# Kernel tuning notes

Hardware: AMD Instinct MI355X
Metric: run time of the kernel (lower is better)

Reference implementation:

```python
import jax, jax.numpy as jnp
import numpy as np

B, S, D, DOM, L = 16, 512, 512, 8, 3  # batch, seq_len, mem_dim (S==D required by outputs*rel), domains, layers


def setup_inputs() -> dict:
    key = jax.random.key(0)
    ks = jax.random.split(key, 16)
    adj = jax.random.uniform(ks[0], (B, S, S), jnp.float32)
    rel = jax.random.uniform(ks[1], (B, S, S), jnp.float32)
    gcn_inputs = jax.random.normal(ks[2], (B, S, D), jnp.float32)
    frontrel = jax.random.normal(ks[3], (B, S, D), jnp.float32)
    backrel = jax.random.normal(ks[4], (B, S, D), jnp.float32)
    # depmap: exactly one selected column per (b, row) so masked_select reshapes to [B,S]
    depmap = jax.nn.one_hot(jax.random.randint(ks[5], (B, S), 0, S), S, dtype=jnp.float32)
    dom_idx = jax.random.randint(ks[6], (B, S), 0, DOM)
    has_dom = jax.random.bernoulli(ks[7], 0.5, (B, S)).astype(jnp.float32)
    domain_id = jax.nn.one_hot(dom_idx, DOM, dtype=jnp.float32) * has_dom[..., None]
    redom_idx = jax.random.randint(ks[8], (B, S), 0, DOM)
    has_re = jax.random.bernoulli(ks[9], 0.5, (B, S)).astype(jnp.float32)
    redomain_id = jax.nn.one_hot(redom_idx, DOM, dtype=jnp.float32) * has_re[..., None]
    domain = jax.random.bernoulli(ks[10], 0.5, (B, S, DOM, 1))
    mask = jnp.ones((B, S), dtype=bool)
    sc = 1.0 / np.sqrt(D)
    W_layers = jax.random.normal(ks[11], (L, D, D), jnp.float32) * sc
    b_layers = jnp.zeros((L, D), jnp.float32)
    prelu_a = jnp.full((L,), 0.25, jnp.float32)  # nn.PReLU default
    W_dg = jax.random.normal(ks[12], (D, D), jnp.float32) * sc
    b_dg = jnp.zeros((D,), jnp.float32)
    W_mg = jax.random.normal(ks[13], (2 * D, D), jnp.float32) * (1.0 / np.sqrt(2 * D))
    b_mg = jnp.zeros((D,), jnp.float32)
    W_out = jax.random.normal(ks[14], (L * D, D), jnp.float32) * (1.0 / np.sqrt(L * D))
    b_out = jnp.zeros((D,), jnp.float32)
    return dict(adj=adj, domain=domain, domain_id=domain_id, redomain_id=redomain_id,
                frontrel=frontrel, backrel=backrel, depmap=depmap, rel=rel,
                gcn_inputs=gcn_inputs, mask=mask, W_layers=W_layers, b_layers=b_layers,
                prelu_a=prelu_a, W_dg=W_dg, b_dg=b_dg, W_mg=W_mg, b_mg=b_mg,
                W_out=W_out, b_out=b_out)


def _forward(adj, domain, domain_id, redomain_id, frontrel, backrel, depmap, rel,
             gcn_inputs, W_layers, b_layers, prelu_a, W_dg, b_dg, W_mg, b_mg, W_out, b_out):
    denom = jnp.sum(adj, axis=2, keepdims=True) + 1.0                     # [B,S,1]
    domain_mask = jnp.sum(domain_id, axis=-1, keepdims=True) == 1.0       # [B,S,1]
    redomain_mask = jnp.sum(redomain_id, axis=-1, keepdims=True) == 1.0   # [B,S,1]
    frontadj = jnp.sum(adj * depmap, axis=-1)                             # [B,S]
    backadj = jnp.sum(jnp.swapaxes(adj, -1, -2) * depmap, axis=-1)        # [B,S]
    outputs = gcn_inputs
    outs = []
    for l in range(L):
        frontoutputs = jnp.where(domain_mask, 0.0, outputs)
        backoutputs = jnp.where(redomain_mask, 0.0, jnp.einsum('bij,bjd->bid', rel, outputs))
        # domain pooling: mask then max over sequence -> [B,DOM,D]
        pooled = jnp.max(jnp.where(domain, -10000.0, outputs[:, :, None, :]), axis=1)
        domain_outputs = jax.nn.sigmoid(pooled @ W_dg + b_dg)             # domain_gate
        frontoutputs = frontoutputs + jnp.einsum('bsk,bkd->bsd', domain_id, domain_outputs)
        backoutputs = backoutputs + jnp.einsum('bsk,bkd->bsd', redomain_id, domain_outputs)
        frontdepadj = jax.nn.sigmoid(jnp.concatenate([frontoutputs, frontrel], -1) @ W_mg + b_mg)
        backdepadj = jax.nn.sigmoid(jnp.concatenate([backoutputs, backrel], -1) @ W_mg + b_mg)
        delta = jnp.einsum('bji,bjd->bid', rel, frontadj[..., None] * frontdepadj * frontoutputs)
        delta = delta + backadj[..., None] * backdepadj * backoutputs
        Ax = jnp.einsum('bij,bjd->bid', adj, outputs * rel)               # requires S==D
        AxW = (Ax @ W_layers[l] + b_layers[l]) + (outputs @ W_layers[l] + b_layers[l]) + delta
        x = AxW / denom
        outputs = jnp.where(x >= 0, x, prelu_a[l] * x)                    # PReLU
        outs.append(outputs)                                              # dropout is eval-mode identity
    gcn_outputs = jnp.concatenate(outs, axis=2)                           # [B,S,L*D]
    return gcn_outputs @ W_out + b_out + gcn_inputs


def reference(adj, domain, domain_id, redomain_id, frontrel, backrel, depmap, rel,
              gcn_inputs, mask, W_layers, b_layers, prelu_a, W_dg, b_dg, W_mg, b_mg,
              W_out, b_out):
    return _forward(adj, domain, domain_id, redomain_id, frontrel, backrel, depmap, rel,
                    gcn_inputs, W_layers, b_layers, prelu_a, W_dg, b_dg, W_mg, b_mg,
                    W_out, b_out)
```

## Files before the change

### kernel.cpp

```cpp
#include <hip/hip_runtime.h>
#include <math.h>

#define SD_  (512*512)
#define BSD_ (16*512*512)

typedef unsigned short u16;
typedef short s16x8 __attribute__((ext_vector_type(8)));
typedef float f32x4 __attribute__((ext_vector_type(4)));

__device__ __forceinline__ float sigmoidf_(float x) { return 1.0f / (1.0f + __expf(-x)); }

__device__ __forceinline__ u16 f2bf(float f) {
    unsigned int u = __float_as_uint(f);
    u += 0x7fffu + ((u >> 16) & 1u);
    return (u16)(u >> 16);
}
__device__ __forceinline__ float bf2f(u16 h) { return __uint_as_float((unsigned)h << 16); }

__device__ __forceinline__ void glds16(const void* g, void* l) {
    __builtin_amdgcn_global_load_lds((const __attribute__((address_space(1))) unsigned int*)g,
                                     (__attribute__((address_space(3))) unsigned int*)l, 16, 0, 0);
}

struct GP {
    const u16 *A1, *A2;  int lda1, lda2;  long sA;
    const u16 *B1, *B2;  int bt1, bt2;  int ldb1, ldb2;  long sB;
    void *C1, *C2;  int obf1, obf2;  int ldc1, ldc2;  long sC;
    const void *Ci1, *Ci2;  int cbf1, cbf2;  int ldci1, ldci2;  long sCi1, sCi2;
    const float *bias;  float bS;
    const float *sc1, *sc2;
    const int *selm1, *seli1, *selm2, *seli2;
    const float *DG;
    const float *invden, *prelu;  int pidx;
    int M, K, zs, swzY;
};

template<int EPI, int ASEL>
__global__ __launch_bounds__(512, 2)
void gemm2(const GP p)
{
    __shared__ short LS[16384];
    const int tid = threadIdx.x;
    int bx, by, bz;
    if (p.swzY >= 0) {
        const int bid = blockIdx.x + 4 * (blockIdx.y + gridDim.y * blockIdx.z);
        const int ppx = (gridDim.y * gridDim.z) >> 3;
        const int xcd = bid & 7, idx = bid >> 3;
        const int pair = xcd * ppx + (idx >> 2);
        bx = idx & 3;
        by = pair & ((1 << p.swzY) - 1);
        bz = pair >> p.swzY;
    } else { bx = blockIdx.x; by = blockIdx.y; bz = blockIdx.z; }

    const int seg = (bz >= p.zs) ? 1 : 0;
    const int z = seg ? bz - p.zs : bz;
    const u16* Ab = (seg ? p.A2 : p.A1) + z * p.sA;
    const int lda = seg ? p.lda2 : p.lda1;
    const u16* Bb = (seg ? p.B2 : p.B1) + z * p.sB;
    const int bt  = seg ? p.bt2  : p.bt1;
    const int ldb = seg ? p.ldb2 : p.ldb1;

    const int m0 = by * 128, n0 = bx * 128;
    const int srow = ((tid >> 6) << 4) | (tid & 15);
    const int sk0 = ((tid >> 4) & 3) << 3;

    int aselv = 0; long dgoff = 0;
    if (ASEL) {
        const int* selm = seg ? p.selm2 : p.selm1;
        const int* seli = seg ? p.seli2 : p.seli1;
        const int row = m0 + srow;
        aselv = selm[row];
        dgoff = (long)((((row) >> 9) << 3) + seli[row]) * 512;
    }
    const u16* aRow = Ab + (long)(m0 + srow) * lda + sk0;
    const u16* bRowT = bt ? (Bb + (long)(n0 + srow) * ldb + sk0) : nullptr;

    auto stage = [&](int kk, int buf) {
        short* lsA = &LS[(buf << 13) + tid * 8];
        short* lsB = lsA + 4096;
        if (ASEL) {
            s16x8 v;
            if (aselv) {
                const float* dg = p.DG + dgoff + kk + sk0;
#pragma unroll
                for (int q = 0; q < 8; ++q) v[q] = (short)f2bf(dg[q]);
            } else v = *(const s16x8*)(aRow + kk);
            *(s16x8*)lsA = v;
        } else {
            glds16(aRow + kk, lsA);
        }
        if (bt) {
            glds16(bRowT + kk, lsB);
        } else {
            s16x8 v;
#pragma unroll
            for (int q = 0; q < 8; ++q) v[q] = (short)Bb[(long)(kk + sk0 + q) * ldb + n0 + srow];
            *(s16x8*)lsB = v;
        }
    };

    const int wave = tid >> 6, lane = tid & 63;
    const int rowSelA = (wave >> 2) << 2;
    const int rowSelB = (wave & 3) << 1;

    f32x4 acc[4][2] = {};
    stage(0, 0);
    const int nkb = p.K >> 5;
    for (int kb = 0; kb < nkb; ++kb) {
        __syncthreads();
        if (kb + 1 < nkb) stage((kb + 1) << 5, (kb + 1) & 1);
        const short* ls = &LS[(kb & 1) << 13];
        s16x8 aF[4], bF[2];
#pragma unroll
        for (int mt = 0; mt < 4; ++mt) aF[mt] = *(const s16x8*)&ls[((rowSelA + mt) * 64 + lane) * 8];
#pragma unroll
        for (int nt = 0; nt < 2; ++nt) bF[nt] = *(const s16x8*)&ls[4096 + ((rowSelB + nt) * 64 + lane) * 8];
#pragma unroll
        for (int mt = 0; mt < 4; ++mt)
#pragma unroll
            for (int nt = 0; nt < 2; ++nt)
                acc[mt][nt] = __builtin_amdgcn_mfma_f32_16x16x32_bf16(aF[mt], bF[nt], acc[mt][nt], 0, 0, 0);
    }

    const int ml = lane & 15, quad = lane >> 4;
    const int wm = (wave >> 2) * 64, wn = (wave & 3) * 32;
    u16* Cb16 = (u16*)(seg ? p.C2 : p.C1);
    float* Cb32 = (float*)(seg ? p.C2 : p.C1);
    const int obf = seg ? p.obf2 : p.obf1;
    const int ldc = seg ? p.ldc2 : p.ldc1;
    if (obf) Cb16 += z * p.sC; else Cb32 += z * p.sC;
    const u16* Ci16 = (const u16*)(seg ? p.Ci2 : p.Ci1);
    const float* Ci32 = (const float*)(seg ? p.Ci2 : p.Ci1);
    const int cbf = seg ? p.cbf2 : p.cbf1;
    const int ldci = seg ? p.ldci2 : p.ldci1;
    {
        const long sCi = seg ? p.sCi2 : p.sCi1;
        if (cbf) Ci16 += z * sCi; else Ci32 += z * sCi;
    }
    const float pal = (EPI == 4) ? p.prelu[p.pidx] : 0.0f;
    const float* scp = (EPI == 8) ? (seg ? p.sc2 : p.sc1) : nullptr;
    const int* eselm = (EPI == 8) ? (seg ? p.selm2 : p.selm1) : nullptr;
    const int* eseli = (EPI == 8) ? (seg ? p.seli2 : p.seli1) : nullptr;

#pragma unroll
    for (int mt = 0; mt < 4; ++mt) {
#pragma unroll
        for (int r = 0; r < 4; ++r) {
            const int row = m0 + wm + mt * 16 + quad * 4 + r;
            float idv = 1.0f, scv = 0.0f; int selv = 0; long dgrow = 0;
            if (EPI == 4) idv = p.invden[z * p.M + row];
            if (EPI == 8) {
                scv = scp[row]; selv = eselm[row];
                dgrow = (long)(((row >> 9) << 3) + eseli[row]) * 512;
            }
            const long crow = (long)row * ldc;
            const long cirow = (long)row * ldci;
#pragma unroll
            for (int nt = 0; nt < 2; ++nt) {
                const int col = n0 + wn + nt * 16 + ml;
                float x = acc[mt][nt][r];
                float cin = 0.0f;
                if (EPI == 3 || EPI == 4 || EPI == 7 || EPI == 8)
                    cin = cbf ? bf2f(Ci16[cirow + col]) : Ci32[cirow + col];
                if (EPI == 1) x += p.bias[col];
                else if (EPI == 3) x += cin;
                else if (EPI == 4) { x = (x + p.bS * p.bias[col] + cin) * idv; x = (x >= 0.0f) ? x : pal * x; }
                else if (EPI == 6) x = sigmoidf_(x + p.bias[col]);
                else if (EPI == 7) x += p.bias[col] + cin;
                else if (EPI == 8) {
                    const float av = selv ? p.DG[dgrow + col] : bf2f(Ab[(long)row * lda + col]);
                    x = sigmoidf_(x + cin) * scv * av;
                }
                if (obf) Cb16[crow + col] = f2bf(x); else Cb32[crow + col] = x;
            }
        }
    }
}

__global__ __launch_bounds__(256)
void cvt_k(const float* __restrict__ s, u16* __restrict__ d)
{
    const long i = ((long)blockIdx.x * 256 + threadIdx.x) * 4;
    const float4 v = *(const float4*)&s[i];
    ushort4 h = { f2bf(v.x), f2bf(v.y), f2bf(v.z), f2bf(v.w) };
    *(ushort4*)&d[i] = h;
}

__global__ __launch_bounds__(256)
void trcvt_k(const float* __restrict__ src, u16* __restrict__ dstT, u16* __restrict__ dstN,
             const int R, const int C, const long sS, const long sDT, const long sDN)
{
    __shared__ u16 t[64][72];
    const float* s = src + blockIdx.z * sS;
    const int r0 = blockIdx.y * 64, c0 = blockIdx.x * 64;
    const int tid = threadIdx.x;
    const int lr = tid >> 2, lc4 = (tid & 3) * 16;
#pragma unroll
    for (int j = 0; j < 4; ++j) {
        const float4 v = *(const float4*)&s[(long)(r0 + lr) * C + c0 + lc4 + j * 4];
        ushort4 h = { f2bf(v.x), f2bf(v.y), f2bf(v.z), f2bf(v.w) };
        *(ushort4*)&t[lr][lc4 + j * 4] = h;
        if (dstN) *(ushort4*)&dstN[blockIdx.z * sDN + (long)(r0 + lr) * C + c0 + lc4 + j * 4] = h;
    }
    __syncthreads();
    const int lcol = tid >> 2, rc = (tid & 3) * 16;
#pragma unroll
    for (int j = 0; j < 2; ++j) {
        s16x8 v;
#pragma unroll
        for (int q = 0; q < 8; ++q) v[q] = (short)t[rc + j * 8 + q][lcol];
        *(s16x8*)&dstT[blockIdx.z * sDT + (long)(c0 + lcol) * R + r0 + rc + j * 8] = v;
    }
}

__global__ __launch_bounds__(256)
void e0_k(const float* __restrict__ adj, const float* __restrict__ depmap,
          const float* __restrict__ domain_id, const float* __restrict__ redomain_id,
          float* __restrict__ invden, float* __restrict__ fa, int* __restrict__ dcol,
          int* __restrict__ dm, int* __restrict__ dsel, int* __restrict__ rm, int* __restrict__ rsel)
{
    const int bs = blockIdx.x;
    const int t = threadIdx.x;
    const float* arow = adj + (long)bs * 512;
    const float* drow = depmap + (long)bs * 512;
    __shared__ float red[256];
    __shared__ int scol;
    if (t == 0) scol = 0;
    const float a0 = arow[t], a1 = arow[t + 256];
    const float p0 = drow[t], p1 = drow[t + 256];
    if (p0 > 0.5f) scol = t;
    if (p1 > 0.5f) scol = t + 256;
    red[t] = a0 + a1;
    __syncthreads();
    for (int off = 128; off > 0; off >>= 1) { if (t < off) red[t] += red[t + off]; __syncthreads(); }
    if (t == 0) invden[bs] = 1.0f / (red[0] + 1.0f);
    __syncthreads();
    red[t] = a0 * p0 + a1 * p1;
    __syncthreads();
    for (int off = 128; off > 0; off >>= 1) { if (t < off) red[t] += red[t + off]; __syncthreads(); }
    if (t == 0) {
        fa[bs] = red[0];
        dcol[bs] = scol;
        const float* q = domain_id + (long)bs * 8;
        float s = 0.f; int sel = 0;
        for (int k = 0; k < 8; ++k) { float v = q[k]; s += v; if (v > 0.5f) sel = k; }
        dm[bs] = (s > 0.5f) ? 1 : 0; dsel[bs] = sel;
        const float* r = redomain_id + (long)bs * 8;
        s = 0.f; sel = 0;
        for (int k = 0; k < 8; ++k) { float v = r[k]; s += v; if (v > 0.5f) sel = k; }
        rm[bs] = (s > 0.5f) ? 1 : 0; rsel[bs] = sel;
    }
}

__global__ void e0b_k(const float* __restrict__ adj, const int* __restrict__ dcol, float* __restrict__ ba)
{
    const int bs = blockIdx.x * 256 + threadIdx.x;
    const int b = bs >> 9, s = bs & 511;
    ba[bs] = adj[((long)b * 512 + dcol[bs]) * 512 + s];
}

__global__ __launch_bounds__(256)
void pool1_k(const u16* __restrict__ OUT, const int ldO, const int* __restrict__ domain,
             const u16* __restrict__ relb, u16* __restrict__ cm, u16* __restrict__ OxRT)
{
    const int b = blockIdx.x >> 4, c = blockIdx.x & 15;
    const int s0 = c * 32, tid = threadIdx.x;
    __shared__ int dom[256];
    dom[tid] = domain[((long)(b * 512 + s0 + (tid >> 3))) * 8 + (tid & 7)];
    __syncthreads();
    const int d0 = tid * 2;
    float mxa[8], mxb[8];
#pragma unroll
    for (int k = 0; k < 8; ++k) { mxa[k] = -10000.0f; mxb[k] = -10000.0f; }
    s16x8 pA[4], pB[4];
#pragma unroll
    for (int s = 0; s < 32; ++s) {
        const int row = b * 512 + s0 + s;
        const unsigned uv = *(const unsigned*)&OUT[(long)row * ldO + d0];
        const unsigned rv = *(const unsigned*)&relb[(long)row * 512 + d0];
        const float vx = bf2f((u16)(uv & 0xffff)), vy = bf2f((u16)(uv >> 16));
        const float rx = bf2f((u16)(rv & 0xffff)), ry = bf2f((u16)(rv >> 16));
        pA[s >> 3][s & 7] = (short)f2bf(vx * rx);
        pB[s >> 3][s & 7] = (short)f2bf(vy * ry);
        const int* ds = &dom[s * 8];
#pragma unroll
        for (int k = 0; k < 8; ++k) {
            mxa[k] = fmaxf(mxa[k], ds[k] ? -10000.0f : vx);
            mxb[k] = fmaxf(mxb[k], ds[k] ? -10000.0f : vy);
        }
    }
#pragma unroll
    for (int j = 0; j < 4; ++j) *(s16x8*)&OxRT[((long)b * 512 + d0) * 512 + s0 + j * 8] = pA[j];
#pragma unroll
    for (int j = 0; j < 4; ++j) *(s16x8*)&OxRT[((long)b * 512 + d0 + 1) * 512 + s0 + j * 8] = pB[j];
#pragma unroll
    for (int k = 0; k < 8; ++k) {
        ushort2 h = { f2bf(mxa[k]), f2bf(mxb[k]) };
        *(ushort2*)&cm[((long)((b * 16 + c) * 8 + k)) * 512 + d0] = h;
    }
}

__global__ void pool2_k(const u16* __restrict__ cm, u16* __restrict__ pooled)
{
    const int q = blockIdx.x * 256 + threadIdx.x;
    const int b = q >> 12, k = (q >> 9) & 7, d = q & 511;
    float m = -1e30f;
    for (int c = 0; c < 16; ++c)
        m = fmaxf(m, bf2f(cm[((long)((b * 16 + c) * 8 + k)) * 512 + d]));
    pooled[((long)(b * 8 + k)) * 512 + d] = f2bf(m);
}

extern "C" void kernel_launch(void* const* d_in, const int* in_sizes, int n_in,
                              void* d_out, int out_size, void* d_ws, size_t ws_size,
                              hipStream_t stream)
{
    const float* adj         = (const float*)d_in[0];
    const int*   domain      = (const int*)d_in[1];
    const float* domain_id   = (const float*)d_in[2];
    const float* redomain_id = (const float*)d_in[3];
    const float* frontrel    = (const float*)d_in[4];
    const float* backrel     = (const float*)d_in[5];
    const float* depmap      = (const float*)d_in[6];
    const float* rel         = (const float*)d_in[7];
    const float* gcn         = (const float*)d_in[8];
    const float* W_layers    = (const float*)d_in[10];
    const float* b_layers    = (const float*)d_in[11];
    const float* prelu_a     = (const float*)d_in[12];
    const float* W_dg        = (const float*)d_in[13];
    const float* b_dg        = (const float*)d_in[14];
    const float* W_mg        = (const float*)d_in[15];
    const float* b_mg        = (const float*)d_in[16];
    const float* W_out       = (const float*)d_in[17];
    const float* b_out       = (const float*)d_in[18];
    float* out = (float*)d_out;

    char* w = (char*)d_ws;
    auto alloc = [&](size_t bytes) { void* p = (void*)w; w += (bytes + 255) & ~(size_t)255; return p; };
    const size_t Bb = (size_t)BSD_ * 2;
    u16* OUTS_bf = (u16*)alloc((size_t)8192 * 1536 * 2);
    u16* RB_bf   = (u16*)alloc(Bb);
    u16* XB_bf   = (u16*)alloc(Bb);
    u16* XF_bf   = (u16*)alloc(Bb);
    u16* OxRT_bf = (u16*)alloc(Bb);
    u16* DL_bf   = (u16*)alloc(Bb);
    u16* AXO_bf  = (u16*)alloc(Bb);
    u16* BB_bf   = (u16*)alloc(Bb);
    u16* FB_bf   = (u16*)alloc(Bb);
    u16* rel_bf  = (u16*)alloc(Bb);
    u16* relT_bf = (u16*)alloc(Bb);
    u16* adj_bf  = (u16*)alloc(Bb);
    u16* gcn_bf  = (u16*)alloc(Bb);
    u16* frel_bf = (u16*)alloc(Bb);
    u16* brel_bf = (u16*)alloc(Bb);
    u16* WmgT1 = (u16*)alloc((size_t)SD_ * 2);
    u16* WmgT2 = (u16*)alloc((size_t)SD_ * 2);
    u16* WdgT  = (u16*)alloc((size_t)SD_ * 2);
    u16* WlT   = (u16*)alloc((size_t)3 * SD_ * 2);
    u16* WoutT = (u16*)alloc((size_t)512 * 1536 * 2);
    u16* cm     = (u16*)alloc((size_t)16 * 16 * 8 * 512 * 2);
    u16* pooled = (u16*)alloc((size_t)16 * 8 * 512 * 2);
    float* DG     = (float*)alloc((size_t)16 * 8 * 512 * 4);
    float* invden = (float*)alloc(8192 * 4);
    float* fa     = (float*)alloc(8192 * 4);
    float* ba     = (float*)alloc(8192 * 4);
    int* dcol = (int*)alloc(8192 * 4);
    int* dm   = (int*)alloc(8192 * 4);
    int* dsel = (int*)alloc(8192 * 4);
    int* rm   = (int*)alloc(8192 * 4);
    int* rsel = (int*)alloc(8192 * 4);

    cvt_k<<<4096, 256, 0, stream>>>(adj, adj_bf);
    cvt_k<<<4096, 256, 0, stream>>>(gcn, gcn_bf);
    cvt_k<<<4096, 256, 0, stream>>>(frontrel, frel_bf);
    cvt_k<<<4096, 256, 0, stream>>>(backrel, brel_bf);
    trcvt_k<<<dim3(8, 8, 16), 256, 0, stream>>>(rel, relT_bf, rel_bf, 512, 512, SD_, SD_, SD_);
    trcvt_k<<<dim3(8, 8, 1), 256, 0, stream>>>(W_mg, WmgT1, nullptr, 512, 512, 0, 0, 0);
    trcvt_k<<<dim3(8, 8, 1), 256, 0, stream>>>(W_mg + SD_, WmgT2, nullptr, 512, 512, 0, 0, 0);
    trcvt_k<<<dim3(8, 8, 1), 256, 0, stream>>>(W_dg, WdgT, nullptr, 512, 512, 0, 0, 0);
    trcvt_k<<<dim3(8, 8, 3), 256, 0, stream>>>(W_layers, WlT, nullptr, 512, 512, SD_, SD_, 0);
    trcvt_k<<<dim3(8, 24, 1), 256, 0, stream>>>(W_out, WoutT, nullptr, 1536, 512, 0, 0, 0);
    e0_k<<<8192, 256, 0, stream>>>(adj, depmap, domain_id, redomain_id, invden, fa, dcol, dm, dsel, rm, rsel);
    e0b_k<<<32, 256, 0, stream>>>(adj, dcol, ba);

    const dim3 blk(512);

    {
        GP p{};
        p.A1 = brel_bf; p.A2 = frel_bf; p.lda1 = p.lda2 = 512; p.sA = 0;
        p.B1 = p.B2 = WmgT2; p.bt1 = p.bt2 = 1; p.ldb1 = p.ldb2 = 512; p.sB = 0;
        p.C1 = BB_bf; p.C2 = FB_bf; p.obf1 = p.obf2 = 1; p.ldc1 = p.ldc2 = 512; p.sC = 0;
        p.bias = b_mg; p.M = 8192; p.K = 512; p.zs = 1; p.swzY = 6;
        gemm2<1, 0><<<dim3(4, 64, 2), blk, 0, stream>>>(p);
    }

    for (int l = 0; l < 3; ++l) {
        const u16* OUTp = (l == 0) ? gcn_bf : (OUTS_bf + (l - 1) * 512);
        const int ldO = (l == 0) ? 512 : 1536;
        const long sO = (long)512 * ldO;

        {
            GP p{};
            p.A1 = rel_bf; p.lda1 = 512; p.sA = SD_;
            p.B1 = OUTp; p.bt1 = 0; p.ldb1 = ldO; p.sB = sO;
            p.C1 = RB_bf; p.obf1 = 1; p.ldc1 = 512; p.sC = SD_;
            p.M = 512; p.K = 512; p.zs = 16; p.swzY = 2;
            gemm2<0, 0><<<dim3(4, 4, 16), blk, 0, stream>>>(p);
        }
        pool1_k<<<256, 256, 0, stream>>>(OUTp, ldO, domain, rel_bf, cm, OxRT_bf);
        pool2_k<<<256, 256, 0, stream>>>(cm, pooled);
        {
            GP p{};
            p.A1 = pooled; p.lda1 = 512; p.B1 = WdgT; p.bt1 = 1; p.ldb1 = 512;
            p.C1 = DG; p.obf1 = 0; p.ldc1 = 512;
            p.bias = b_dg; p.M = 128; p.K = 512; p.zs = 1; p.swzY = -1;
            gemm2<6, 0><<<dim3(4, 1, 1), blk, 0, stream>>>(p);
        }
        {
            GP p{};
            p.A1 = RB_bf; p.lda1 = 512; p.A2 = OUTp; p.lda2 = ldO; p.sA = 0;
            p.selm1 = rm; p.seli1 = rsel; p.selm2 = dm; p.seli2 = dsel; p.DG = DG;
            p.B1 = p.B2 = WmgT1; p.bt1 = p.bt2 = 1; p.ldb1 = p.ldb2 = 512; p.sB = 0;
            p.Ci1 = BB_bf; p.Ci2 = FB_bf; p.cbf1 = p.cbf2 = 1; p.ldci1 = p.ldci2 = 512; p.sCi1 = p.sCi2 = 0;
            p.C1 = XB_bf; p.C2 = XF_bf; p.obf1 = p.obf2 = 1; p.ldc1 = p.ldc2 = 512; p.sC = 0;
            p.sc1 = ba; p.sc2 = fa; p.M = 8192; p.K = 512; p.zs = 1; p.swzY = 6;
            gemm2<8, 1><<<dim3(4, 64, 2), blk, 0, stream>>>(p);
        }
        {
            GP p{};
            p.A1 = relT_bf; p.lda1 = 512; p.A2 = adj_bf; p.lda2 = 512; p.sA = SD_;
            p.B1 = XF_bf; p.bt1 = 0; p.ldb1 = 512;
            p.B2 = OxRT_bf; p.bt2 = 1; p.ldb2 = 512; p.sB = SD_;
            p.Ci1 = XB_bf; p.cbf1 = 1; p.ldci1 = 512; p.sCi1 = SD_;
            p.Ci2 = OUTp; p.cbf2 = 1; p.ldci2 = ldO; p.sCi2 = sO;
            p.C1 = DL_bf; p.C2 = AXO_bf; p.obf1 = p.obf2 = 1; p.ldc1 = p.ldc2 = 512; p.sC = SD_;
            p.M = 512; p.K = 512; p.zs = 16; p.swzY = 2;
            gemm2<3, 0><<<dim3(4, 4, 32), blk, 0, stream>>>(p);
        }
        {
            GP p{};
            p.A1 = AXO_bf; p.lda1 = 512; p.sA = SD_;
            p.B1 = WlT + (long)l * SD_; p.bt1 = 1; p.ldb1 = 512; p.sB = 0;
            p.Ci1 = DL_bf; p.cbf1 = 1; p.ldci1 = 512; p.sCi1 = SD_;
            p.C1 = OUTS_bf + l * 512; p.obf1 = 1; p.ldc1 = 1536; p.sC = (long)512 * 1536;
            p.bias = b_layers + l * 512; p.bS = 2.0f;
            p.invden = invden; p.prelu = prelu_a; p.pidx = l;
            p.M = 512; p.K = 512; p.zs = 16; p.swzY = 2;
            gemm2<4, 0><<<dim3(4, 4, 16), blk, 0, stream>>>(p);
        }
    }

    {
        GP p{};
        p.A1 = OUTS_bf; p.lda1 = 1536; p.sA = 0;
        p.B1 = WoutT; p.bt1 = 1; p.ldb1 = 1536; p.sB = 0;
        p.Ci1 = gcn; p.cbf1 = 0; p.ldci1 = 512; p.sCi1 = 0;
        p.C1 = out; p.obf1 = 0; p.ldc1 = 512; p.sC = 0;
        p.bias = b_out; p.M = 8192; p.K = 1536; p.zs = 1; p.swzY = 6;
        gemm2<7, 0><<<dim3(4, 64, 1), blk, 0, stream>>>(p);
    }
}
```

Measured before the change: 712.1 us.

## Write transposed GEMM outputs so all B operands load via direct LDS

```diff
diff --git a/kernel.cpp b/kernel.cpp
--- a/kernel.cpp
+++ b/kernel.cpp
@@ -24,30 +24,31 @@
 
 struct GP {
     const u16 *A1, *A2;  int lda1, lda2;  long sA;
-    const u16 *B1, *B2;  int bt1, bt2;  int ldb1, ldb2;  long sB;
-    void *C1, *C2;  int obf1, obf2;  int ldc1, ldc2;  long sC;
-    const void *Ci1, *Ci2;  int cbf1, cbf2;  int ldci1, ldci2;  long sCi1, sCi2;
+    const u16 *B1, *B2;  int ldb1, ldb2;  long sB;
+    void *C1, *C2;  int obf1, obf2, ldc1, ldc2;  long sC;
+    u16 *CT1, *CT2;  int ldcT1, ldcT2;  long sCT;
+    const void *Ci1, *Ci2;  int cbf1, cbf2, ldci1, ldci2;  long sCi1, sCi2;
     const float *bias;  float bS;
     const float *sc1, *sc2;
     const int *selm1, *seli1, *selm2, *seli2;
     const float *DG;
     const float *invden, *prelu;  int pidx;
-    int M, K, zs, swzY;
+    int M, K, zs, swzX, swzY;
 };
 
-template<int EPI, int ASEL>
-__global__ __launch_bounds__(512, 2)
+template<int EPI, int ASEL, int TRW>
+__global__ __launch_bounds__(256, 4)
 void gemm2(const GP p)
 {
-    __shared__ short LS[16384];
+    __shared__ short LS[12288];
     const int tid = threadIdx.x;
     int bx, by, bz;
-    if (p.swzY >= 0) {
-        const int bid = blockIdx.x + 4 * (blockIdx.y + gridDim.y * blockIdx.z);
+    if (p.swzX >= 0) {
+        const int bid = blockIdx.x + gridDim.x * (blockIdx.y + gridDim.y * blockIdx.z);
         const int ppx = (gridDim.y * gridDim.z) >> 3;
         const int xcd = bid & 7, idx = bid >> 3;
-        const int pair = xcd * ppx + (idx >> 2);
-        bx = idx & 3;
+        const int pair = xcd * ppx + (idx >> p.swzX);
+        bx = idx & ((1 << p.swzX) - 1);
         by = pair & ((1 << p.swzY) - 1);
         bz = pair >> p.swzY;
     } else { bx = blockIdx.x; by = blockIdx.y; bz = blockIdx.z; }
@@ -57,51 +58,49 @@
     const u16* Ab = (seg ? p.A2 : p.A1) + z * p.sA;
     const int lda = seg ? p.lda2 : p.lda1;
     const u16* Bb = (seg ? p.B2 : p.B1) + z * p.sB;
-    const int bt  = seg ? p.bt2  : p.bt1;
     const int ldb = seg ? p.ldb2 : p.ldb1;
 
-    const int m0 = by * 128, n0 = bx * 128;
+    const int m0 = by * 128, n0 = bx * 64;
     const int srow = ((tid >> 6) << 4) | (tid & 15);
     const int sk0 = ((tid >> 4) & 3) << 3;
 
-    int aselv = 0; long dgoff = 0;
+    const u16* aRow0 = Ab + (long)(m0 + srow) * lda + sk0;
+    const u16* aRow1 = aRow0 + (long)64 * lda;
+    const u16* bRow  = Bb + (long)(n0 + srow) * ldb + sk0;
+
+    int aselv0 = 0, aselv1 = 0; long dgo0 = 0, dgo1 = 0;
     if (ASEL) {
         const int* selm = seg ? p.selm2 : p.selm1;
         const int* seli = seg ? p.seli2 : p.seli1;
-        const int row = m0 + srow;
-        aselv = selm[row];
-        dgoff = (long)((((row) >> 9) << 3) + seli[row]) * 512;
-    }
-    const u16* aRow = Ab + (long)(m0 + srow) * lda + sk0;
-    const u16* bRowT = bt ? (Bb + (long)(n0 + srow) * ldb + sk0) : nullptr;
+        const int r0 = m0 + srow, r1 = r0 + 64;
+        aselv0 = selm[r0]; dgo0 = (long)(((r0 >> 9) << 3) + seli[r0]) * 512 + sk0;
+        aselv1 = selm[r1]; dgo1 = (long)(((r1 >> 9) << 3) + seli[r1]) * 512 + sk0;
+    }
 
     auto stage = [&](int kk, int buf) {
-        short* lsA = &LS[(buf << 13) + tid * 8];
-        short* lsB = lsA + 4096;
+        short* base = &LS[buf * 6144];
         if (ASEL) {
-            s16x8 v;
-            if (aselv) {
-                const float* dg = p.DG + dgoff + kk + sk0;
-#pragma unroll
-                for (int q = 0; q < 8; ++q) v[q] = (short)f2bf(dg[q]);
-            } else v = *(const s16x8*)(aRow + kk);
-            *(s16x8*)lsA = v;
+            s16x8 v0, v1;
+            if (aselv0) { const float* dg = p.DG + dgo0 + kk;
+#pragma unroll
+                for (int q = 0; q < 8; ++q) v0[q] = (short)f2bf(dg[q]); }
+            else v0 = *(const s16x8*)(aRow0 + kk);
+            if (aselv1) { const float* dg = p.DG + dgo1 + kk;
+#pragma unroll
+                for (int q = 0; q < 8; ++q) v1[q] = (short)f2bf(dg[q]); }
+            else v1 = *(const s16x8*)(aRow1 + kk);
+            *(s16x8*)&base[tid * 8] = v0;
+            *(s16x8*)&base[2048 + tid * 8] = v1;
         } else {
-            glds16(aRow + kk, lsA);
-        }
-        if (bt) {
-            glds16(bRowT + kk, lsB);
-        } else {
-            s16x8 v;
-#pragma unroll
-            for (int q = 0; q < 8; ++q) v[q] = (short)Bb[(long)(kk + sk0 + q) * ldb + n0 + srow];
-            *(s16x8*)lsB = v;
-        }
+            glds16(aRow0 + kk, &base[tid * 8]);
+            glds16(aRow1 + kk, &base[2048 + tid * 8]);
+        }
+        glds16(bRow + kk, &base[4096 + tid * 8]);
     };
 
     const int wave = tid >> 6, lane = tid & 63;
-    const int rowSelA = (wave >> 2) << 2;
-    const int rowSelB = (wave & 3) << 1;
+    const int rowSelA = (wave >> 1) << 2;
+    const int rowSelB = (wave & 1) << 1;
 
     f32x4 acc[4][2] = {};
     stage(0, 0);
@@ -109,7 +108,7 @@
     for (int kb = 0; kb < nkb; ++kb) {
         __syncthreads();
         if (kb + 1 < nkb) stage((kb + 1) << 5, (kb + 1) & 1);
-        const short* ls = &LS[(kb & 1) << 13];
+        const short* ls = &LS[(kb & 1) * 6144];
         s16x8 aF[4], bF[2];
 #pragma unroll
         for (int mt = 0; mt < 4; ++mt) aF[mt] = *(const s16x8*)&ls[((rowSelA + mt) * 64 + lane) * 8];
@@ -123,12 +122,16 @@
     }
 
     const int ml = lane & 15, quad = lane >> 4;
-    const int wm = (wave >> 2) * 64, wn = (wave & 3) * 32;
+    const int wm = (wave >> 1) * 64, wn = (wave & 1) * 32;
     u16* Cb16 = (u16*)(seg ? p.C2 : p.C1);
     float* Cb32 = (float*)(seg ? p.C2 : p.C1);
+    const int haveC = (seg ? p.C2 : p.C1) != nullptr;
     const int obf = seg ? p.obf2 : p.obf1;
     const int ldc = seg ? p.ldc2 : p.ldc1;
-    if (obf) Cb16 += z * p.sC; else Cb32 += z * p.sC;
+    if (haveC) { if (obf) Cb16 += z * p.sC; else Cb32 += z * p.sC; }
+    u16* CTb = (TRW ? (seg ? p.CT2 : p.CT1) : nullptr);
+    const int ldcT = seg ? p.ldcT2 : p.ldcT1;
+    if (TRW && CTb) CTb += z * p.sCT;
     const u16* Ci16 = (const u16*)(seg ? p.Ci2 : p.Ci1);
     const float* Ci32 = (const float*)(seg ? p.Ci2 : p.Ci1);
     const int cbf = seg ? p.cbf2 : p.cbf1;
@@ -145,33 +148,37 @@
 #pragma unroll
     for (int mt = 0; mt < 4; ++mt) {
 #pragma unroll
-        for (int r = 0; r < 4; ++r) {
-            const int row = m0 + wm + mt * 16 + quad * 4 + r;
-            float idv = 1.0f, scv = 0.0f; int selv = 0; long dgrow = 0;
-            if (EPI == 4) idv = p.invden[z * p.M + row];
-            if (EPI == 8) {
-                scv = scp[row]; selv = eselm[row];
-                dgrow = (long)(((row >> 9) << 3) + eseli[row]) * 512;
-            }
-            const long crow = (long)row * ldc;
-            const long cirow = (long)row * ldci;
-#pragma unroll
-            for (int nt = 0; nt < 2; ++nt) {
-                const int col = n0 + wn + nt * 16 + ml;
+        for (int nt = 0; nt < 2; ++nt) {
+            const int col = n0 + wn + nt * 16 + ml;
+            u16 pk[4];
+#pragma unroll
+            for (int r = 0; r < 4; ++r) {
+                const int row = m0 + wm + mt * 16 + quad * 4 + r;
                 float x = acc[mt][nt][r];
                 float cin = 0.0f;
                 if (EPI == 3 || EPI == 4 || EPI == 7 || EPI == 8)
-                    cin = cbf ? bf2f(Ci16[cirow + col]) : Ci32[cirow + col];
+                    cin = cbf ? bf2f(Ci16[(long)row * ldci + col]) : Ci32[(long)row * ldci + col];
                 if (EPI == 1) x += p.bias[col];
                 else if (EPI == 3) x += cin;
-                else if (EPI == 4) { x = (x + p.bS * p.bias[col] + cin) * idv; x = (x >= 0.0f) ? x : pal * x; }
+                else if (EPI == 4) {
+                    x = (x + p.bS * p.bias[col] + cin) * p.invden[z * p.M + row];
+                    x = (x >= 0.0f) ? x : pal * x;
+                }
                 else if (EPI == 6) x = sigmoidf_(x + p.bias[col]);
                 else if (EPI == 7) x += p.bias[col] + cin;
                 else if (EPI == 8) {
-                    const float av = selv ? p.DG[dgrow + col] : bf2f(Ab[(long)row * lda + col]);
-                    x = sigmoidf_(x + cin) * scv * av;
+                    float av;
+                    if (eselm[row]) av = p.DG[(long)(((row >> 9) << 3) + eseli[row]) * 512 + col];
+                    else av = bf2f(Ab[(long)row * lda + col]);
+                    x = sigmoidf_(x + cin) * scp[row] * av;
                 }
-                if (obf) Cb16[crow + col] = f2bf(x); else Cb32[crow + col] = x;
+                if (haveC) { if (obf) Cb16[(long)row * ldc + col] = f2bf(x); else Cb32[(long)row * ldc + col] = x; }
+                pk[r] = f2bf(x);
+            }
+            if (TRW && CTb) {
+                const int mrow = m0 + wm + mt * 16 + quad * 4;
+                u16* ct = CTb + ((long)(mrow >> 9)) * p.sCT + (long)col * ldcT + (mrow & 511);
+                *(ushort4*)ct = *(ushort4*)pk;
             }
         }
     }
@@ -338,9 +345,11 @@
     auto alloc = [&](size_t bytes) { void* p = (void*)w; w += (bytes + 255) & ~(size_t)255; return p; };
     const size_t Bb = (size_t)BSD_ * 2;
     u16* OUTS_bf = (u16*)alloc((size_t)8192 * 1536 * 2);
+    u16* OUTT    = (u16*)alloc(Bb);
+    u16* gcnT    = (u16*)alloc(Bb);
     u16* RB_bf   = (u16*)alloc(Bb);
     u16* XB_bf   = (u16*)alloc(Bb);
-    u16* XF_bf   = (u16*)alloc(Bb);
+    u16* XFT_bf  = (u16*)alloc(Bb);
     u16* OxRT_bf = (u16*)alloc(Bb);
     u16* DL_bf   = (u16*)alloc(Bb);
     u16* AXO_bf  = (u16*)alloc(Bb);
@@ -370,9 +379,9 @@
     int* rsel = (int*)alloc(8192 * 4);
 
     cvt_k<<<4096, 256, 0, stream>>>(adj, adj_bf);
-    cvt_k<<<4096, 256, 0, stream>>>(gcn, gcn_bf);
     cvt_k<<<4096, 256, 0, stream>>>(frontrel, frel_bf);
     cvt_k<<<4096, 256, 0, stream>>>(backrel, brel_bf);
+    trcvt_k<<<dim3(8, 8, 16), 256, 0, stream>>>(gcn, gcnT, gcn_bf, 512, 512, SD_, SD_, SD_);
     trcvt_k<<<dim3(8, 8, 16), 256, 0, stream>>>(rel, relT_bf, rel_bf, 512, 512, SD_, SD_, SD_);
     trcvt_k<<<dim3(8, 8, 1), 256, 0, stream>>>(W_mg, WmgT1, nullptr, 512, 512, 0, 0, 0);
     trcvt_k<<<dim3(8, 8, 1), 256, 0, stream>>>(W_mg + SD_, WmgT2, nullptr, 512, 512, 0, 0, 0);
@@ -382,80 +391,83 @@
     e0_k<<<8192, 256, 0, stream>>>(adj, depmap, domain_id, redomain_id, invden, fa, dcol, dm, dsel, rm, rsel);
     e0b_k<<<32, 256, 0, stream>>>(adj, dcol, ba);
 
-    const dim3 blk(512);
+    const dim3 blk(256);
 
     {
         GP p{};
         p.A1 = brel_bf; p.A2 = frel_bf; p.lda1 = p.lda2 = 512; p.sA = 0;
-        p.B1 = p.B2 = WmgT2; p.bt1 = p.bt2 = 1; p.ldb1 = p.ldb2 = 512; p.sB = 0;
+        p.B1 = p.B2 = WmgT2; p.ldb1 = p.ldb2 = 512; p.sB = 0;
         p.C1 = BB_bf; p.C2 = FB_bf; p.obf1 = p.obf2 = 1; p.ldc1 = p.ldc2 = 512; p.sC = 0;
-        p.bias = b_mg; p.M = 8192; p.K = 512; p.zs = 1; p.swzY = 6;
-        gemm2<1, 0><<<dim3(4, 64, 2), blk, 0, stream>>>(p);
+        p.bias = b_mg; p.M = 8192; p.K = 512; p.zs = 1; p.swzX = 3; p.swzY = 6;
+        gemm2<1, 0, 0><<<dim3(8, 64, 2), blk, 0, stream>>>(p);
     }
 
     for (int l = 0; l < 3; ++l) {
-        const u16* OUTp = (l == 0) ? gcn_bf : (OUTS_bf + (l - 1) * 512);
+        const u16* OUTp  = (l == 0) ? gcn_bf : (OUTS_bf + (l - 1) * 512);
+        const u16* OUTTp = (l == 0) ? gcnT : OUTT;
         const int ldO = (l == 0) ? 512 : 1536;
         const long sO = (long)512 * ldO;
 
         {
             GP p{};
             p.A1 = rel_bf; p.lda1 = 512; p.sA = SD_;
-            p.B1 = OUTp; p.bt1 = 0; p.ldb1 = ldO; p.sB = sO;
+            p.B1 = OUTTp; p.ldb1 = 512; p.sB = SD_;
             p.C1 = RB_bf; p.obf1 = 1; p.ldc1 = 512; p.sC = SD_;
-            p.M = 512; p.K = 512; p.zs = 16; p.swzY = 2;
-            gemm2<0, 0><<<dim3(4, 4, 16), blk, 0, stream>>>(p);
+            p.M = 512; p.K = 512; p.zs = 16; p.swzX = 3; p.swzY = 2;
+            gemm2<0, 0, 0><<<dim3(8, 4, 16), blk, 0, stream>>>(p);
         }
         pool1_k<<<256, 256, 0, stream>>>(OUTp, ldO, domain, rel_bf, cm, OxRT_bf);
         pool2_k<<<256, 256, 0, stream>>>(cm, pooled);
         {
             GP p{};
-            p.A1 = pooled; p.lda1 = 512; p.B1 = WdgT; p.bt1 = 1; p.ldb1 = 512;
+            p.A1 = pooled; p.lda1 = 512; p.B1 = WdgT; p.ldb1 = 512;
             p.C1 = DG; p.obf1 = 0; p.ldc1 = 512;
-            p.bias = b_dg; p.M = 128; p.K = 512; p.zs = 1; p.swzY = -1;
-            gemm2<6, 0><<<dim3(4, 1, 1), blk, 0, stream>>>(p);
+            p.bias = b_dg; p.M = 128; p.K = 512; p.zs = 1; p.swzX = -1;
+            gemm2<6, 0, 0><<<dim3(8, 1, 1), blk, 0, stream>>>(p);
         }
         {
             GP p{};
             p.A1 = RB_bf; p.lda1 = 512; p.A2 = OUTp; p.lda2 = ldO; p.sA = 0;
             p.selm1 = rm; p.seli1 = rsel; p.selm2 = dm; p.seli2 = dsel; p.DG = DG;
-            p.B1 = p.B2 = WmgT1; p.bt1 = p.bt2 = 1; p.ldb1 = p.ldb2 = 512; p.sB = 0;
+            p.B1 = p.B2 = WmgT1; p.ldb1 = p.ldb2 = 512; p.sB = 0;
             p.Ci1 = BB_bf; p.Ci2 = FB_bf; p.cbf1 = p.cbf2 = 1; p.ldci1 = p.ldci2 = 512; p.sCi1 = p.sCi2 = 0;
-            p.C1 = XB_bf; p.C2 = XF_bf; p.obf1 = p.obf2 = 1; p.ldc1 = p.ldc2 = 512; p.sC = 0;
-            p.sc1 = ba; p.sc2 = fa; p.M = 8192; p.K = 512; p.zs = 1; p.swzY = 6;
-            gemm2<8, 1><<<dim3(4, 64, 2), blk, 0, stream>>>(p);
+            p.C1 = XB_bf; p.C2 = nullptr; p.obf1 = 1; p.ldc1 = 512; p.sC = 0;
+            p.CT1 = nullptr; p.CT2 = XFT_bf; p.ldcT2 = 512; p.sCT = SD_;
+            p.sc1 = ba; p.sc2 = fa; p.M = 8192; p.K = 512; p.zs = 1; p.swzX = 3; p.swzY = 6;
+            gemm2<8, 1, 1><<<dim3(8, 64, 2), blk, 0, stream>>>(p);
         }
         {
             GP p{};
             p.A1 = relT_bf; p.lda1 = 512; p.A2 = adj_bf; p.lda2 = 512; p.sA = SD_;
-            p.B1 = XF_bf; p.bt1 = 0; p.ldb1 = 512;
-            p.B2 = OxRT_bf; p.bt2 = 1; p.ldb2 = 512; p.sB = SD_;
+            p.B1 = XFT_bf; p.ldb1 = 512;
+            p.B2 = OxRT_bf; p.ldb2 = 512; p.sB = SD_;
             p.Ci1 = XB_bf; p.cbf1 = 1; p.ldci1 = 512; p.sCi1 = SD_;
             p.Ci2 = OUTp; p.cbf2 = 1; p.ldci2 = ldO; p.sCi2 = sO;
             p.C1 = DL_bf; p.C2 = AXO_bf; p.obf1 = p.obf2 = 1; p.ldc1 = p.ldc2 = 512; p.sC = SD_;
-            p.M = 512; p.K = 512; p.zs = 16; p.swzY = 2;
-            gemm2<3, 0><<<dim3(4, 4, 32), blk, 0, stream>>>(p);
+            p.M = 512; p.K = 512; p.zs = 16; p.swzX = 3; p.swzY = 2;
+            gemm2<3, 0, 0><<<dim3(8, 4, 32), blk, 0, stream>>>(p);
         }
         {
             GP p{};
             p.A1 = AXO_bf; p.lda1 = 512; p.sA = SD_;
-            p.B1 = WlT + (long)l * SD_; p.bt1 = 1; p.ldb1 = 512; p.sB = 0;
+            p.B1 = WlT + (long)l * SD_; p.ldb1 = 512; p.sB = 0;
             p.Ci1 = DL_bf; p.cbf1 = 1; p.ldci1 = 512; p.sCi1 = SD_;
             p.C1 = OUTS_bf + l * 512; p.obf1 = 1; p.ldc1 = 1536; p.sC = (long)512 * 1536;
+            p.CT1 = OUTT; p.ldcT1 = 512; p.sCT = SD_;
             p.bias = b_layers + l * 512; p.bS = 2.0f;
             p.invden = invden; p.prelu = prelu_a; p.pidx = l;
-            p.M = 512; p.K = 512; p.zs = 16; p.swzY = 2;
-            gemm2<4, 0><<<dim3(4, 4, 16), blk, 0, stream>>>(p);
+            p.M = 512; p.K = 512; p.zs = 16; p.swzX = 3; p.swzY = 2;
+            gemm2<4, 0, 1><<<dim3(8, 4, 16), blk, 0, stream>>>(p);
         }
     }
 
     {
         GP p{};
         p.A1 = OUTS_bf; p.lda1 = 1536; p.sA = 0;
-        p.B1 = WoutT; p.bt1 = 1; p.ldb1 = 1536; p.sB = 0;
+        p.B1 = WoutT; p.ldb1 = 1536; p.sB = 0;
         p.Ci1 = gcn; p.cbf1 = 0; p.ldci1 = 512; p.sCi1 = 0;
         p.C1 = out; p.obf1 = 0; p.ldc1 = 512; p.sC = 0;
-        p.bias = b_out; p.M = 8192; p.K = 1536; p.zs = 1; p.swzY = 6;
-        gemm2<7, 0><<<dim3(4, 64, 1), blk, 0, stream>>>(p);
-    }
-}
+        p.bias = b_out; p.M = 8192; p.K = 1536; p.zs = 1; p.swzX = 3; p.swzY = 6;
+        gemm2<7, 0, 0><<<dim3(8, 64, 1), blk, 0, stream>>>(p);
+    }
+}
```

After: 817.5 us. 1.15x slower.
